# Optimization experiments

Hardware: AMD Instinct MI355X
Metric: run time of the kernel (lower is better)

Reference implementation:

```python
import jax, jax.numpy as jnp
import numpy as np

K = 20  # number of top neighbors kept per row
NOISE_SCALE = 1e-4


def setup_inputs() -> dict:
    key = jax.random.key(0)
    k1, k2 = jax.random.split(key)
    B, N = 16, 2048
    A = jax.random.normal(k1, (B, N, N), dtype=jnp.float32)
    noise = jax.random.uniform(k2, (B, N, N), dtype=jnp.float32)
    return {"A": A, "noise": noise}


def reference(A, noise):
    # _activate: ReLU
    A = jax.nn.relu(A)

    # _sparsify: per-row top-k on noise-doped scores, scatter a 0/1 mask, multiply
    A_doped = A + noise * NOISE_SCALE
    _, topk_idx = jax.lax.top_k(A_doped, K)  # (B, N, K)
    B, N, _ = A.shape
    b_idx = jnp.arange(B)[:, None, None]
    r_idx = jnp.arange(N)[None, :, None]
    mask = jnp.zeros_like(A).at[b_idx, r_idx, topk_idx].set(1.0)
    A = A * mask

    # _symmetrize
    A = (A + jnp.swapaxes(A, 1, 2)) * 0.5

    # _normalize ('sym'): A <- D^{-1/2} (A + I) D^{-1/2}
    A = A + jnp.eye(N, dtype=A.dtype)
    d_inv = jnp.sum(A, axis=2) ** -0.5  # (B, N)
    d_inv = jnp.where(jnp.isinf(d_inv), 0.0, d_inv)
    # diag(d) @ A @ diag(d) expressed via broadcasting (same math as batched matmul)
    A = d_inv[:, :, None] * A * d_inv[:, None, :]
    return A
```

## Files before the change

kernel.cpp:

```cpp
#include <hip/hip_runtime.h>

#define NN 2048
#define KK 20
#define BB 16
#define TPRE 1.79989f
#define CAP 128
#define CSLOT 64

typedef __attribute__((ext_vector_type(4))) float f32x4;

__global__ __launch_bounds__(256) void topk_kernel(
    const float* __restrict__ A, const float* __restrict__ noise,
    int* __restrict__ sel_idx, float* __restrict__ sel_val,
    float* __restrict__ colsum, int* __restrict__ col_cnt,
    unsigned short* __restrict__ col_src)
{
    __shared__ unsigned long long cand_pk[4][CAP + 8];
    __shared__ float cand_val[4][CAP];
    __shared__ int   cand_idx[4][CAP];
    __shared__ int   tie_idx[4][64];
    __shared__ int   tie_cnt[4];

    const int lane = threadIdx.x & 63;
    const int wv   = threadIdx.x >> 6;
    const int row  = blockIdx.x * 4 + wv;
    const float* Ar = A     + (size_t)row * NN;
    const float* Nr = noise + (size_t)row * NN;
    const int colbase = row & ~(NN - 1);
    const unsigned long long ltm = (1ull << lane) - 1ull;

    int*   si = sel_idx + (size_t)row * KK;
    float* sv = sel_val + (size_t)row * KK;

#define EMIT(POS, IDX, V)                                                      \
    do {                                                                       \
        int _p = (POS); int _i = (IDX); float _v = (V);                        \
        si[_p] = _i; sv[_p] = _v;                                              \
        atomicAdd(&colsum[colbase + _i], _v);                                  \
        int _s = atomicAdd(&col_cnt[colbase + _i], 1);                         \
        if (_s < CSLOT)                                                        \
            col_src[(size_t)(colbase + _i) * CSLOT + _s] =                     \
                (unsigned short)(((row & (NN - 1)) << 5) | _p);                \
    } while (0)

    float4 a[8];
#pragma unroll
    for (int c = 0; c < 8; ++c)
        a[c] = *(const float4*)(Ar + c * 256 + lane * 4);

    int cnt = 0;
#pragma unroll
    for (int c = 0; c < 8; ++c) {
        float av[4] = {a[c].x, a[c].y, a[c].z, a[c].w};
#pragma unroll
        for (int q = 0; q < 4; ++q) {
            float v = fmaxf(av[q], 0.f);
            bool p = v >= TPRE;
            unsigned long long m = __ballot(p);
            if (p) {
                int pos = cnt + __popcll(m & ltm);
                if (pos < CAP) {
                    cand_val[wv][pos] = v;
                    cand_idx[wv][pos] = c * 256 + lane * 4 + q;
                }
            }
            cnt += __popcll(m);
        }
    }

    bool done = false;
    if (cnt >= KK && cnt <= CAP) {
        int   i0 = (lane      < cnt) ? cand_idx[wv][lane]      : -1;
        int   i1 = (lane + 64 < cnt) ? cand_idx[wv][lane + 64] : -1;
        float v0 = (i0 >= 0) ? cand_val[wv][lane]      : 0.f;
        float v1 = (i1 >= 0) ? cand_val[wv][lane + 64] : 0.f;
        unsigned long long pk0 = ~0ull, pk1 = ~0ull;
        if (i0 >= 0) {
            float k0 = fmaf(Nr[i0], 1e-4f, v0);
            pk0 = ((unsigned long long)__float_as_uint(k0) << 32)
                | (unsigned)(NN - 1 - i0);
            cand_pk[wv][lane] = pk0;
        }
        if (i1 >= 0) {
            float k1 = fmaf(Nr[i1], 1e-4f, v1);
            pk1 = ((unsigned long long)__float_as_uint(k1) << 32)
                | (unsigned)(NN - 1 - i1);
            cand_pk[wv][lane + 64] = pk1;
        }
        int nIter = (cnt + 7) & ~7;
        if (lane < nIter - cnt) cand_pk[wv][cnt + lane] = 0ull;

        int r0 = 0, r1 = 0;
        for (int j = 0; j < nIter; j += 8) {
            unsigned long long b[8];
#pragma unroll
            for (int u = 0; u < 8; ++u) b[u] = cand_pk[wv][j + u];
#pragma unroll
            for (int u = 0; u < 8; ++u) {
                r0 += (b[u] > pk0);
                r1 += (b[u] > pk1);
            }
        }
        if (i0 >= 0 && r0 < KK) EMIT(r0, i0, v0);
        if (i1 >= 0 && r1 < KK) EMIT(r1, i1, v1);
        done = true;
    }

    if (!done) {
        unsigned lo = 0u, hi = 0x7F800000u;
        unsigned tb = 0u;
        bool exact = false;
        while (hi - lo > 1u) {
            unsigned mid = (lo + hi) >> 1;
            float tm = __uint_as_float(mid);
            int c = 0;
            for (int j = 0; j < 32; ++j) {
                float av = Ar[j * 64 + lane];
                float nv = Nr[j * 64 + lane];
                float k = fmaf(nv, 1e-4f, fmaxf(av, 0.f));
                c += __popcll(__ballot(k >= tm));
            }
            if (c == KK) { tb = mid; exact = true; break; }
            if (c > KK) lo = mid; else hi = mid;
        }
        if (exact) {
            float t = __uint_as_float(tb);
            int run = 0;
            for (int j = 0; j < 32; ++j) {
                float av = Ar[j * 64 + lane];
                float nv = Nr[j * 64 + lane];
                float v = fmaxf(av, 0.f);
                float k = fmaf(nv, 1e-4f, v);
                bool p = k >= t;
                unsigned long long m = __ballot(p);
                if (p) EMIT(run + __popcll(m & ltm), j * 64 + lane, v);
                run += __popcll(m);
            }
        } else {
            float t1 = __uint_as_float(lo);
            int run = 0;
            for (int j = 0; j < 32; ++j) {
                float av = Ar[j * 64 + lane];
                float nv = Nr[j * 64 + lane];
                float v = fmaxf(av, 0.f);
                float k = fmaf(nv, 1e-4f, v);
                bool p = k > t1;
                unsigned long long m = __ballot(p);
                if (p) EMIT(run + __popcll(m & ltm), j * 64 + lane, v);
                run += __popcll(m);
            }
            if (lane == 0) tie_cnt[wv] = 0;
            for (int j = 0; j < 32; ++j) {
                float av = Ar[j * 64 + lane];
                float nv = Nr[j * 64 + lane];
                float k = fmaf(nv, 1e-4f, fmaxf(av, 0.f));
                if (k == t1) {
                    int p = atomicAdd(&tie_cnt[wv], 1);
                    if (p < 64) tie_idx[wv][p] = j * 64 + lane;
                }
            }
            if (lane == 0) {
                int n = tie_cnt[wv]; if (n > 64) n = 64;
                int need = KK - run;
                for (int s = 0; s < need; ++s) {
                    int bq = 0, bidx = 0x7fffffff;
                    for (int q = 0; q < n; ++q) {
                        int v = tie_idx[wv][q];
                        if (v < bidx) { bidx = v; bq = q; }
                    }
                    tie_idx[wv][bq] = 0x7fffffff;
                    float v = fmaxf(Ar[bidx], 0.f);
                    EMIT(run + s, bidx, v);
                }
            }
        }
    }
#undef EMIT
}

__global__ __launch_bounds__(256) void dinv_kernel(
    const float* __restrict__ sel_val, const float* __restrict__ colsum,
    float* __restrict__ dinv)
{
    int r = blockIdx.x * 256 + threadIdx.x;
    const float* svp = sel_val + (size_t)r * KK;
    float rs = 0.f;
#pragma unroll
    for (int k = 0; k < KK; ++k) rs += svp[k];
    float d = 1.0f + 0.5f * (rs + colsum[r]);
    dinv[r] = 1.0f / sqrtf(d);
}

__global__ __launch_bounds__(256) void dense_row_kernel(
    const int* __restrict__ sel_idx, const float* __restrict__ sel_val,
    const int* __restrict__ col_cnt, const unsigned short* __restrict__ col_src,
    const float* __restrict__ dinv, float* __restrict__ out)
{
    __shared__ float rowbuf[NN];
    const int r = blockIdx.x;
    const int i = r & (NN - 1);
    const int t = threadIdx.x;
    const int colbase = r & ~(NN - 1);

    float4 z = {0.f, 0.f, 0.f, 0.f};
#pragma unroll
    for (int c = 0; c < 2; ++c)
        *(float4*)(rowbuf + c * 1024 + t * 4) = z;
    __syncthreads();

    float di = dinv[r];
    if (t == 0) atomicAdd(&rowbuf[i], di * di);
    if (t < KK) {
        int j  = sel_idx[(size_t)r * KK + t];
        float v = sel_val[(size_t)r * KK + t];
        atomicAdd(&rowbuf[j], 0.5f * v * di * dinv[colbase + j]);
    }
    int cnt = col_cnt[r]; if (cnt > CSLOT) cnt = CSLOT;
    if (t < cnt) {
        unsigned short pk = col_src[(size_t)r * CSLOT + t];
        int srow = pk >> 5, k = pk & 31;
        float v = sel_val[(size_t)(colbase + srow) * KK + k];
        atomicAdd(&rowbuf[srow], 0.5f * v * di * dinv[colbase + srow]);
    }
    __syncthreads();

    size_t base = (size_t)r * NN;
#pragma unroll
    for (int c = 0; c < 2; ++c) {
        int col = c * 1024 + t * 4;
        *(float4*)(out + base + col) = *(const float4*)(rowbuf + col);
    }
}

extern "C" void kernel_launch(void* const* d_in, const int* in_sizes, int n_in,
                              void* d_out, int out_size, void* d_ws, size_t ws_size,
                              hipStream_t stream)
{
    const float* A     = (const float*)d_in[0];
    const float* noise = (const float*)d_in[1];
    float* out = (float*)d_out;
    char*  ws  = (char*)d_ws;

    const int rows = BB * NN;
    size_t off = 0;
    int*   sel_idx = (int*)(ws + off);            off += (size_t)rows * KK * 4;
    float* sel_val = (float*)(ws + off);          off += (size_t)rows * KK * 4;
    float* colsum  = (float*)(ws + off);          off += (size_t)rows * 4;
    float* dinv    = (float*)(ws + off);          off += (size_t)rows * 4;
    int*   col_cnt = (int*)(ws + off);            off += (size_t)rows * 4;
    unsigned short* col_src = (unsigned short*)(ws + off);

    hipMemsetAsync(colsum, 0, rows * sizeof(float), stream);
    hipMemsetAsync(col_cnt, 0, rows * sizeof(int), stream);

    topk_kernel<<<rows / 4, 256, 0, stream>>>(A, noise, sel_idx, sel_val,
                                              colsum, col_cnt, col_src);
    dinv_kernel<<<rows / 256, 256, 0, stream>>>(sel_val, colsum, dinv);
    dense_row_kernel<<<rows, 256, 0, stream>>>(sel_idx, sel_val, col_cnt,
                                               col_src, dinv, out);
}
```

Measured before the change: 635.8 us.

## Replace dense row assembly with output memset plus global atomic scatter

The output is now zeroed with a device memset, and a new scatter kernel writes each selected edge into both symmetric positions, plus the diagonal, using global atomicAdd. This removes the per-column source lists (col_cnt/col_src) and their atomics from the top-k kernel. It also drops the LDS-buffered per-row dense write kernel. It trades a fused zero-and-write pass for a memset plus scattered atomics into a large buffer, and it removes the CSLOT overflow cap.

```diff
diff --git a/kernel.cpp b/kernel.cpp
--- a/kernel.cpp
+++ b/kernel.cpp
@@ -5,15 +5,13 @@
 #define BB 16
 #define TPRE 1.79989f
 #define CAP 128
-#define CSLOT 64
 
 typedef __attribute__((ext_vector_type(4))) float f32x4;
 
 __global__ __launch_bounds__(256) void topk_kernel(
     const float* __restrict__ A, const float* __restrict__ noise,
     int* __restrict__ sel_idx, float* __restrict__ sel_val,
-    float* __restrict__ colsum, int* __restrict__ col_cnt,
-    unsigned short* __restrict__ col_src)
+    float* __restrict__ colsum)
 {
     __shared__ unsigned long long cand_pk[4][CAP + 8];
     __shared__ float cand_val[4][CAP];
@@ -37,10 +35,6 @@
         int _p = (POS); int _i = (IDX); float _v = (V);                        \
         si[_p] = _i; sv[_p] = _v;                                              \
         atomicAdd(&colsum[colbase + _i], _v);                                  \
-        int _s = atomicAdd(&col_cnt[colbase + _i], 1);                         \
-        if (_s < CSLOT)                                                        \
-            col_src[(size_t)(colbase + _i) * CSLOT + _s] =                     \
-                (unsigned short)(((row & (NN - 1)) << 5) | _p);                \
     } while (0)
 
     float4 a[8];
@@ -191,44 +185,25 @@
     dinv[r] = 1.0f / sqrtf(d);
 }
 
-__global__ __launch_bounds__(256) void dense_row_kernel(
+__global__ __launch_bounds__(256) void scatter_kernel(
     const int* __restrict__ sel_idx, const float* __restrict__ sel_val,
-    const int* __restrict__ col_cnt, const unsigned short* __restrict__ col_src,
     const float* __restrict__ dinv, float* __restrict__ out)
 {
-    __shared__ float rowbuf[NN];
-    const int r = blockIdx.x;
+    int tid = blockIdx.x * 256 + threadIdx.x;
+    int r = tid / 21;
+    int s = tid - r * 21;
+    const int colbase = r & ~(NN - 1);
     const int i = r & (NN - 1);
-    const int t = threadIdx.x;
-    const int colbase = r & ~(NN - 1);
-
-    float4 z = {0.f, 0.f, 0.f, 0.f};
-#pragma unroll
-    for (int c = 0; c < 2; ++c)
-        *(float4*)(rowbuf + c * 1024 + t * 4) = z;
-    __syncthreads();
-
-    float di = dinv[r];
-    if (t == 0) atomicAdd(&rowbuf[i], di * di);
-    if (t < KK) {
-        int j  = sel_idx[(size_t)r * KK + t];
-        float v = sel_val[(size_t)r * KK + t];
-        atomicAdd(&rowbuf[j], 0.5f * v * di * dinv[colbase + j]);
-    }
-    int cnt = col_cnt[r]; if (cnt > CSLOT) cnt = CSLOT;
-    if (t < cnt) {
-        unsigned short pk = col_src[(size_t)r * CSLOT + t];
-        int srow = pk >> 5, k = pk & 31;
-        float v = sel_val[(size_t)(colbase + srow) * KK + k];
-        atomicAdd(&rowbuf[srow], 0.5f * v * di * dinv[colbase + srow]);
-    }
-    __syncthreads();
-
-    size_t base = (size_t)r * NN;
-#pragma unroll
-    for (int c = 0; c < 2; ++c) {
-        int col = c * 1024 + t * 4;
-        *(float4*)(out + base + col) = *(const float4*)(rowbuf + col);
+    float dr = dinv[r];
+
+    if (s == 20) {
+        atomicAdd(&out[(size_t)r * NN + i], dr * dr);
+    } else {
+        int   j = sel_idx[(size_t)r * KK + s];
+        float v = sel_val[(size_t)r * KK + s];
+        float w = 0.5f * v * dr * dinv[colbase + j];
+        atomicAdd(&out[(size_t)r * NN + j], w);
+        atomicAdd(&out[(size_t)(colbase + j) * NN + i], w);
     }
 }
 
@@ -246,16 +221,12 @@
     int*   sel_idx = (int*)(ws + off);            off += (size_t)rows * KK * 4;
     float* sel_val = (float*)(ws + off);          off += (size_t)rows * KK * 4;
     float* colsum  = (float*)(ws + off);          off += (size_t)rows * 4;
-    float* dinv    = (float*)(ws + off);          off += (size_t)rows * 4;
-    int*   col_cnt = (int*)(ws + off);            off += (size_t)rows * 4;
-    unsigned short* col_src = (unsigned short*)(ws + off);
-
+    float* dinv    = (float*)(ws + off);
+
+    hipMemsetAsync(out, 0, (size_t)out_size, stream);
     hipMemsetAsync(colsum, 0, rows * sizeof(float), stream);
-    hipMemsetAsync(col_cnt, 0, rows * sizeof(int), stream);
-
-    topk_kernel<<<rows / 4, 256, 0, stream>>>(A, noise, sel_idx, sel_val,
-                                              colsum, col_cnt, col_src);
+
+    topk_kernel<<<rows / 4, 256, 0, stream>>>(A, noise, sel_idx, sel_val, colsum);
     dinv_kernel<<<rows / 256, 256, 0, stream>>>(sel_val, colsum, dinv);
-    dense_row_kernel<<<rows, 256, 0, stream>>>(sel_idx, sel_val, col_cnt,
-                                               col_src, dinv, out);
-}
+    scatter_kernel<<<rows * 21 / 256, 256, 0, stream>>>(sel_idx, sel_val, dinv, out);
+}
```

After: 619.5 us. 2.6% less time.
